# Optimization experiments

Measured on AMD Instinct MI355X. Metric: run time of the kernel, lower is better.

Reference implementation:

```python
import jax, jax.numpy as jnp
import numpy as np

B, N, H, DH, ORDER, DEG = 64, 256, 8, 64, 4, 16
D = H * DH
TOTAL = B * N
E = TOTAL * DEG


def setup_inputs() -> dict:
    key = jax.random.key(0)
    ks = jax.random.split(key, 16)
    output = jax.random.normal(ks[0], (N, B, D), dtype=jnp.float32)
    # attention weights: positive, row-normalized like softmax output
    attn = jax.nn.softmax(jax.random.normal(ks[1], (B, H, N, N), dtype=jnp.float32), axis=-1)
    out_each_head = jax.random.normal(ks[2], (B, N, H, DH), dtype=jnp.float32)
    # random graph edges, endpoints within the same graph (global node ids)
    g = jax.random.randint(ks[3], (E,), 0, B)
    s = g * N + jax.random.randint(ks[4], (E,), 0, N)
    d = g * N + jax.random.randint(ks[5], (E,), 0, N)
    edge_index = jnp.stack([s, d], axis=0).astype(jnp.int64)
    # full graphs, no padding: feature_indices[:,0]=graph id, [:,1]=node pos
    fi = jnp.stack([jnp.repeat(jnp.arange(B), N), jnp.tile(jnp.arange(N), B)], axis=1).astype(jnp.int64)
    batch = fi[:, 0]
    sc = 0.1
    params = dict(
        W_gcn=jax.random.normal(ks[6], (ORDER, ORDER)) * sc,
        b_gcn=jnp.zeros((ORDER,), jnp.float32),
        W_lin=jax.random.normal(ks[7], (ORDER, ORDER)) * sc,
        b_lin=jnp.zeros((ORDER,), jnp.float32),
        W_cheb=jax.random.normal(ks[8], (ORDER, DH, DH)) * sc,
        b_cheb=jnp.zeros((DH,), jnp.float32),
        W_cat=jax.random.normal(ks[9], (2 * D, D)) * sc,
        b_cat=jnp.zeros((D,), jnp.float32),
        gamma=jnp.ones((D,), jnp.float32),
        beta=jnp.zeros((D,), jnp.float32),
    )
    return dict(output=output, attn=attn, out_each_head=out_each_head,
                edge_index=edge_index, feature_indices=fi, batch=batch, **params)


def reference(output, attn, out_each_head, edge_index, feature_indices, batch,
              W_gcn, b_gcn, W_lin, b_lin, W_cheb, b_cheb, W_cat, b_cat, gamma, beta):
    Bn, Hn, Nn, _ = attn.shape
    C = W_gcn.shape[0]
    total = Bn * Nn
    NT = Hn * total

    # ---- get_filter_coefficients: GCN over fully-connected attention graphs ----
    # edge weights are detached in the original (edge_weight.detach())
    A = jax.lax.stop_gradient(attn).transpose(1, 0, 2, 3).reshape(Hn * Bn, Nn, Nn)
    A_hat = A + jnp.eye(Nn, dtype=A.dtype)  # add self loops (weight 1)
    deg = A_hat.sum(axis=1)                 # deg_j = sum_i A_hat[i,j]
    dinv = jnp.where(deg > 0, jax.lax.rsqrt(deg), 0.0)  # (HB, N)
    # x = ones, so x @ W_gcn is a constant row = column sums of W_gcn
    w_row = W_gcn.sum(axis=0)               # (C,)
    s = jnp.einsum('bi,bij->bj', dinv, A_hat) * dinv     # (HB, N)
    x_c = jnp.tanh(s[:, :, None] * w_row + b_gcn)        # (HB, N, C)
    gap = x_c.mean(axis=1)                  # global avg pool per graph (HB, C)
    coeff = gap @ W_lin + b_lin             # (HB, C) rows ordered (head, batch)

    # ---- dynamic Chebyshev filtering per head on the input graph ----
    offsets = (jnp.arange(Hn) * total).astype(edge_index.dtype)
    src = (edge_index[0][None, :] + offsets[:, None]).reshape(-1)
    dst = (edge_index[1][None, :] + offsets[:, None]).reshape(-1)
    deg_n = jax.ops.segment_sum(jnp.ones(src.shape[0], jnp.float32), dst, num_segments=NT)
    dinv_n = jnp.where(deg_n > 0, jax.lax.rsqrt(deg_n), 0.0)
    norm_e = -(dinv_n[src] * dinv_n[dst])   # scaled Laplacian L_hat = -D^-1/2 A D^-1/2

    def prop(x):  # L_hat @ x via gather/scatter
        return jax.ops.segment_sum(norm_e[:, None] * x[src], dst, num_segments=NT)

    # nodes ordered (head, batch, node)
    x0 = out_each_head.transpose(2, 0, 1, 3).reshape(NT, DH)
    batch_all = (batch[None, :] + (jnp.arange(Hn) * Bn)[:, None]).reshape(-1)  # graph id h*B+b
    c_node = coeff[batch_all]               # (NT, ORDER) per-node dynamic coefficients

    T_prev, T_cur = x0, prop(x0)
    acc = c_node[:, 0:1] * (T_prev @ W_cheb[0]) + c_node[:, 1:2] * (T_cur @ W_cheb[1])
    for k in range(2, C):
        T_next = 2.0 * prop(T_cur) - T_prev
        acc = acc + c_node[:, k:k + 1] * (T_next @ W_cheb[k])
        T_prev, T_cur = T_cur, T_next
    acc = acc + b_cheb                      # (NT, DH)

    # regroup heads: (H, B*N, DH) -> (B*N, H*DH), scatter back to (N, B, D)
    filtered = acc.reshape(Hn, total, DH).transpose(1, 0, 2).reshape(total, Hn * DH)
    out_filtered = jnp.zeros_like(output).at[feature_indices[:, 1], feature_indices[:, 0], :].set(filtered)

    # skip connection + linear_cat + final LayerNorm
    out_cat = jnp.concatenate([output, out_filtered], axis=-1)
    out = out_cat @ W_cat + b_cat
    mu = out.mean(axis=-1, keepdims=True)
    var = ((out - mu) ** 2).mean(axis=-1, keepdims=True)
    out = (out - mu) * jax.lax.rsqrt(var + 1e-5) * gamma + beta
    return out
```

## Files before the change

kernel.cpp:

```cpp
#include <hip/hip_runtime.h>
#include <stdint.h>

#define Bq      64
#define Nq      256
#define Hq      8
#define DHq     64
#define TOTALq  16384
#define NTq     131072
#define Dq      512

typedef __attribute__((ext_vector_type(8))) short short8;
typedef __attribute__((ext_vector_type(4))) float floatx4;

__device__ __forceinline__ unsigned short f2bf(float f) {
    union { float f; unsigned int u; } c; c.f = f;
    unsigned int u = c.u;
    return (unsigned short)((u + 0x7fffu + ((u >> 16) & 1u)) >> 16);
}
__device__ __forceinline__ float bf2f(unsigned short u) {
    union { unsigned int u; float f; } c; c.u = ((unsigned int)u) << 16;
    return c.f;
}

__global__ void pscatter_kernel(const int* __restrict__ srcp, const int* __restrict__ dstp,
                                const int* __restrict__ cnt, float* __restrict__ Pf, int E) {
    int e = blockIdx.x * 256 + threadIdx.x;
    if (e >= E) return;
    int s = srcp[e], d = dstp[e];
    int cs = cnt[s], cd = cnt[d];
    float dvs = (cs > 0) ? rsqrtf((float)cs) : 0.0f;
    float dvd = (cd > 0) ? rsqrtf((float)cd) : 0.0f;
    int g = d >> 8;
    atomicAdd(&Pf[((size_t)g << 16) + ((size_t)(d & 255) << 8) + (s & 255)],
              -(dvs * dvd));
}

__global__ void pconv_kernel(const float* __restrict__ Pf, unsigned short* __restrict__ Pb) {
    int i = (blockIdx.x * 256 + threadIdx.x) * 4;
    float4 v = *(const float4*)(Pf + i);
    unsigned int lo = (unsigned int)f2bf(v.x) | ((unsigned int)f2bf(v.y) << 16);
    unsigned int hi = (unsigned int)f2bf(v.z) | ((unsigned int)f2bf(v.w) << 16);
    *(uint2*)(Pb + i) = make_uint2(lo, hi);
}

__global__ __launch_bounds__(512, 1)
void front_kernel(const float* __restrict__ attn,
                  const float* __restrict__ Wg, const float* __restrict__ bg,
                  const float* __restrict__ Wlin, const float* __restrict__ blin,
                  float* __restrict__ coeff,
                  const int* __restrict__ dstp, int* __restrict__ cnt, int E,
                  const float* __restrict__ Wcat, unsigned short* __restrict__ Wt2,
                  const float* __restrict__ Wch, float* __restrict__ WchTf,
                  float* __restrict__ Pf) {
    __shared__ floatx4 part[8][64];
    __shared__ floatx4 dinv4[64];
    const int bid = blockIdx.x;
    const int tid = threadIdx.x;

    if (bid < 512) {
        const int g = bid;
        const int h = g >> 6;
        const int b = g & 63;
        const float* A = attn + ((size_t)(b * Hq + h)) * (Nq * Nq);
        const int rg = tid >> 6;
        const int cv = tid & 63;
        const float* Ap = A + cv * 4;

        floatx4 regs[32];
        floatx4 s1 = (floatx4){0.f, 0.f, 0.f, 0.f};
#pragma unroll
        for (int r = 0; r < 32; ++r) {
            regs[r] = *(const floatx4*)(Ap + (size_t)(rg * 32 + r) * 256);
            s1 += regs[r];
        }
        part[rg][cv] = s1;
        __syncthreads();

        if (tid < 64) {
            floatx4 cs = part[0][tid];
#pragma unroll
            for (int i = 1; i < 8; ++i) cs += part[i][tid];
            floatx4 dv;
#pragma unroll
            for (int i = 0; i < 4; ++i) dv[i] = rsqrtf(cs[i] + 1.0f);
            dinv4[tid] = dv;
        }
        __syncthreads();

        const float* dsc = (const float*)dinv4;
        floatx4 s2 = (floatx4){0.f, 0.f, 0.f, 0.f};
#pragma unroll
        for (int r = 0; r < 32; ++r)
            s2 += dsc[rg * 32 + r] * regs[r];
        part[rg][cv] = s2;
        __syncthreads();

        if (tid < 64) {
            floatx4 ws = part[0][tid];
#pragma unroll
            for (int i = 1; i < 8; ++i) ws += part[i][tid];
            floatx4 dv = dinv4[tid];
            floatx4 sj = (ws + dv) * dv;

            float wr[4], bgl[4];
#pragma unroll
            for (int c = 0; c < 4; ++c) {
                wr[c]  = Wg[0 * 4 + c] + Wg[1 * 4 + c] + Wg[2 * 4 + c] + Wg[3 * 4 + c];
                bgl[c] = bg[c];
            }
            float v[4];
#pragma unroll
            for (int c = 0; c < 4; ++c) {
                v[c] = tanhf(sj[0] * wr[c] + bgl[c]) + tanhf(sj[1] * wr[c] + bgl[c]) +
                       tanhf(sj[2] * wr[c] + bgl[c]) + tanhf(sj[3] * wr[c] + bgl[c]);
#pragma unroll
                for (int o = 32; o >= 1; o >>= 1) v[c] += __shfl_down(v[c], o, 64);
            }
            float g0 = __shfl(v[0], 0, 64), g1 = __shfl(v[1], 0, 64);
            float g2 = __shfl(v[2], 0, 64), g3 = __shfl(v[3], 0, 64);
            if (tid < 4) {
                float r = blin[tid] + (g0 * Wlin[0 * 4 + tid] + g1 * Wlin[1 * 4 + tid] +
                                       g2 * Wlin[2 * 4 + tid] + g3 * Wlin[3 * 4 + tid]) *
                                          (1.0f / 256.0f);
                coeff[g * 4 + tid] = r;
            }
        }
        return;
    }

    const int nbCnt = (E + 511) >> 9;
    if (bid < 512 + nbCnt) {
        int e = (bid - 512) * 512 + tid;
        if (e < E) atomicAdd(&cnt[dstp[e]], 1);
        return;
    }
    if (bid < 512 + nbCnt + 160) {
        int pb = bid - 512 - nbCnt;
        if (pb < 128) {
            int idx = pb * 512 + tid;
            int col = idx & 511;
            int ktq = idx >> 9;
            const float* src = Wcat + (size_t)(ktq * 8) * 512 + col;
            unsigned int pk[4];
#pragma unroll
            for (int q2 = 0; q2 < 4; ++q2) {
                unsigned short a = f2bf(src[(q2 * 2 + 0) * 512]);
                unsigned short b = f2bf(src[(q2 * 2 + 1) * 512]);
                pk[q2] = (unsigned int)a | ((unsigned int)b << 16);
            }
            *(uint4*)(Wt2 + (size_t)idx * 8) = make_uint4(pk[0], pk[1], pk[2], pk[3]);
        } else {
            int idx = (pb - 128) * 512 + tid;
            int k = idx >> 12, rem = idx & 4095;
            int n = rem >> 6, j = rem & 63;
            WchTf[idx] = Wch[(k << 12) + (j << 6) + n];
        }
        return;
    }
    {
        int zb = bid - 512 - nbCnt - 160;
        size_t i = ((size_t)zb * 512 + tid) * 4;
        *(float4*)(Pf + i) = make_float4(0.f, 0.f, 0.f, 0.f);
    }
}

__global__ __launch_bounds__(512, 2)
void cheb_fused(const unsigned short* __restrict__ Pb, const float* __restrict__ oeh,
                const float* __restrict__ WchTf, const float* __restrict__ coeff,
                const float* __restrict__ bch, unsigned short* __restrict__ filtb) {
    extern __shared__ unsigned char sm[];
    unsigned short* cm = (unsigned short*)sm;
    unsigned short* rm = (unsigned short*)(sm + 32768);
    unsigned short* Wl = (unsigned short*)(sm + 65536);

    const int g = blockIdx.x;
    const int b = (g & 7) * 8 + ((g >> 3) & 7);
    const int h = g >> 6;
    const int tid = threadIdx.x;
    const int lane = tid & 63, wv = tid >> 6;
    const int wr = wv >> 1, wc = wv & 1;
    const int quad = lane >> 4, l15 = lane & 15;

    const unsigned short* Pbase = Pb + ((size_t)b << 16);
    const float* cf = coeff + (h * 64 + b) * 4;

    {
        const int sn = tid >> 1;
        const int sh = (tid & 1) * 32;
        const float* sp = oeh + (size_t)(b * 256 + sn) * 512 + h * 64 + sh;
        unsigned int pk[16];
#pragma unroll
        for (int j = 0; j < 8; ++j) {
            float4 v = *(const float4*)(sp + j * 4);
            pk[2 * j]     = (unsigned)f2bf(v.x) | ((unsigned)f2bf(v.y) << 16);
            pk[2 * j + 1] = (unsigned)f2bf(v.z) | ((unsigned)f2bf(v.w) << 16);
        }
#pragma unroll
        for (int jj = 0; jj < 4; ++jj)
            *(uint4*)(rm + sn * 64 + ((((sh >> 3) + jj) ^ (sn & 7)) << 3)) =
                make_uint4(pk[4 * jj], pk[4 * jj + 1], pk[4 * jj + 2], pk[4 * jj + 3]);
#pragma unroll
        for (int e = 0; e < 32; ++e) {
            int c = sh + e;
            unsigned short v =
                (unsigned short)((e & 1) ? (pk[e >> 1] >> 16) : (pk[e >> 1] & 0xffffu));
            cm[c * 256 + (((sn >> 3) ^ (c & 31)) << 3) + (sn & 7)] = v;
        }
        float ck = cf[0];
        int r = tid >> 3, su = tid & 7;
        const float* wp = WchTf + r * 64 + su * 8;
        float4 w0 = *(const float4*)wp, w1 = *(const float4*)(wp + 4);
        *(uint4*)(Wl + r * 72 + su * 8) = make_uint4(
            (unsigned)f2bf(w0.x * ck) | ((unsigned)f2bf(w0.y * ck) << 16),
            (unsigned)f2bf(w0.z * ck) | ((unsigned)f2bf(w0.w * ck) << 16),
            (unsigned)f2bf(w1.x * ck) | ((unsigned)f2bf(w1.y * ck) << 16),
            (unsigned)f2bf(w1.z * ck) | ((unsigned)f2bf(w1.w * ck) << 16));
    }
    __syncthreads();

    unsigned int curp[4][2][2], prvp[4][2][2];
#pragma unroll
    for (int rt = 0; rt < 4; ++rt)
#pragma unroll
        for (int ct = 0; ct < 2; ++ct)
#pragma unroll
            for (int p = 0; p < 2; ++p) {
                int m = wr * 64 + rt * 16 + quad * 4 + 2 * p;
                int c = wc * 32 + ct * 16 + l15;
                curp[rt][ct][p] = *(const unsigned int*)(cm + c * 256 +
                                                         (((m >> 3) ^ (c & 31)) << 3) + (m & 7));
                prvp[rt][ct][p] = 0u;
            }

    floatx4 accf[4][2];
#pragma unroll
    for (int rt = 0; rt < 4; ++rt)
#pragma unroll
        for (int ct = 0; ct < 2; ++ct) accf[rt][ct] = (floatx4){0.f, 0.f, 0.f, 0.f};

#pragma unroll
    for (int k = 0; k < 4; ++k) {
#pragma unroll
        for (int kk = 0; kk < 2; ++kk) {
            short8 af[4], bfw[2];
#pragma unroll
            for (int rt = 0; rt < 4; ++rt) {
                int row = wr * 64 + rt * 16 + l15;
                af[rt] = *(const short8*)(rm + row * 64 + (((kk * 4 + quad) ^ (row & 7)) << 3));
            }
#pragma unroll
            for (int ct = 0; ct < 2; ++ct) {
                int oc = wc * 32 + ct * 16 + l15;
                bfw[ct] = *(const short8*)(Wl + oc * 72 + kk * 32 + quad * 8);
            }
#pragma unroll
            for (int rt = 0; rt < 4; ++rt)
#pragma unroll
                for (int ct = 0; ct < 2; ++ct)
                    accf[rt][ct] = __builtin_amdgcn_mfma_f32_16x16x32_bf16(
                        af[rt], bfw[ct], accf[rt][ct], 0, 0, 0);
        }
        if (k < 3) {
            floatx4 accp[4][2];
#pragma unroll
            for (int rt = 0; rt < 4; ++rt)
#pragma unroll
                for (int ct = 0; ct < 2; ++ct) accp[rt][ct] = (floatx4){0.f, 0.f, 0.f, 0.f};
#pragma unroll
            for (int kt = 0; kt < 8; ++kt) {
                short8 ap[4], bp[2];
#pragma unroll
                for (int rt = 0; rt < 4; ++rt) {
                    int row = wr * 64 + rt * 16 + l15;
                    ap[rt] = *(const short8*)(Pbase + row * 256 + kt * 32 + quad * 8);
                }
#pragma unroll
                for (int ct = 0; ct < 2; ++ct) {
                    int c = wc * 32 + ct * 16 + l15;
                    bp[ct] = *(const short8*)(cm + c * 256 + (((kt * 4 + quad) ^ (c & 31)) << 3));
                }
#pragma unroll
                for (int rt = 0; rt < 4; ++rt)
#pragma unroll
                    for (int ct = 0; ct < 2; ++ct)
                        accp[rt][ct] = __builtin_amdgcn_mfma_f32_16x16x32_bf16(
                            ap[rt], bp[ct], accp[rt][ct], 0, 0, 0);
            }
            __syncthreads();
#pragma unroll
            for (int rt = 0; rt < 4; ++rt)
#pragma unroll
                for (int ct = 0; ct < 2; ++ct)
#pragma unroll
                    for (int p = 0; p < 2; ++p) {
                        float a0 = accp[rt][ct][2 * p], a1 = accp[rt][ct][2 * p + 1];
                        if (k > 0) {
                            unsigned pv = prvp[rt][ct][p];
                            a0 = 2.0f * a0 - bf2f((unsigned short)(pv & 0xffffu));
                            a1 = 2.0f * a1 - bf2f((unsigned short)(pv >> 16));
                        }
                        unsigned nv = (unsigned)f2bf(a0) | ((unsigned)f2bf(a1) << 16);
                        prvp[rt][ct][p] = curp[rt][ct][p];
                        curp[rt][ct][p] = nv;
                        int m = wr * 64 + rt * 16 + quad * 4 + 2 * p;
                        int c = wc * 32 + ct * 16 + l15;
                        if (k < 2)
                            *(unsigned int*)(cm + c * 256 + (((m >> 3) ^ (c & 31)) << 3) +
                                             (m & 7)) = nv;
                        rm[m * 64 + (((c >> 3) ^ (m & 7)) << 3) + (c & 7)] =
                            (unsigned short)(nv & 0xffffu);
                        rm[(m + 1) * 64 + (((c >> 3) ^ ((m + 1) & 7)) << 3) + (c & 7)] =
                            (unsigned short)(nv >> 16);
                    }
            {
                float ck = cf[k + 1];
                int r = tid >> 3, su = tid & 7;
                const float* wp = WchTf + (k + 1) * 4096 + r * 64 + su * 8;
                float4 w0 = *(const float4*)wp, w1 = *(const float4*)(wp + 4);
                *(uint4*)(Wl + r * 72 + su * 8) = make_uint4(
                    (unsigned)f2bf(w0.x * ck) | ((unsigned)f2bf(w0.y * ck) << 16),
                    (unsigned)f2bf(w0.z * ck) | ((unsigned)f2bf(w0.w * ck) << 16),
                    (unsigned)f2bf(w1.x * ck) | ((unsigned)f2bf(w1.y * ck) << 16),
                    (unsigned)f2bf(w1.z * ck) | ((unsigned)f2bf(w1.w * ck) << 16));
            }
            __syncthreads();
        }
    }

    float bias[2];
#pragma unroll
    for (int ct = 0; ct < 2; ++ct) bias[ct] = bch[wc * 32 + ct * 16 + l15];
#pragma unroll
    for (int rt = 0; rt < 4; ++rt)
#pragma unroll
        for (int ct = 0; ct < 2; ++ct) {
            int c = wc * 32 + ct * 16 + l15;
#pragma unroll
            for (int i = 0; i < 4; ++i) {
                int m = wr * 64 + rt * 16 + quad * 4 + i;
                filtb[((size_t)m * 64 + b) * 512 + h * 64 + c] =
                    f2bf(accf[rt][ct][i] + bias[ct]);
            }
        }
}

__global__ __launch_bounds__(512, 2)
void gemm_ln_mfma(const float* __restrict__ outp, const unsigned short* __restrict__ filtb,
                  const unsigned short* __restrict__ Wt2, const float* __restrict__ bcat,
                  const float* __restrict__ gamma, const float* __restrict__ beta,
                  float* __restrict__ out) {
    extern __shared__ unsigned char smc[];
    unsigned short* A_lds0 = (unsigned short*)smc;
    unsigned short* A_lds1 = (unsigned short*)(smc + 4096);
    float* ep = (float*)smc;

    const int tid = threadIdx.x;
    const int lane = tid & 63;
    const int wv = tid >> 6;
    const int quad = lane >> 4;
    const int l15 = lane & 15;
    const int r0 = blockIdx.x * 64;

    const int s_row = tid >> 3;
    const int s_sub = tid & 7;
    const int s_q   = s_sub >> 1;
    const int s_e   = (s_sub & 1) * 4;

    const size_t boff = (size_t)(quad * 512 + wv * 64 + l15) * 8;

    floatx4 acc[4][4];
#pragma unroll
    for (int rt = 0; rt < 4; ++rt)
#pragma unroll
        for (int ct = 0; ct < 4; ++ct) acc[rt][ct] = (floatx4){0.f, 0.f, 0.f, 0.f};

    short8 bA[4], bB[4];
    float4 avX_f, avY_f;
    uint2  avX_b, avY_b;

    {
#pragma unroll
        for (int ct = 0; ct < 4; ++ct)
            bA[ct] = *(const short8*)(Wt2 + boff + ct * 128);
#pragma unroll
        for (int ct = 0; ct < 4; ++ct)
            bB[ct] = *(const short8*)(Wt2 + (size_t)16384 + boff + ct * 128);
        float4 av = *(const float4*)(outp + (size_t)(r0 + s_row) * 512 + s_sub * 4);
        avY_f = *(const float4*)(outp + (size_t)(r0 + s_row) * 512 + 32 + s_sub * 4);
        uint2 ap;
        ap.x = (unsigned int)f2bf(av.x) | ((unsigned int)f2bf(av.y) << 16);
        ap.y = (unsigned int)f2bf(av.z) | ((unsigned int)f2bf(av.w) << 16);
        *(uint2*)(A_lds0 + (s_q * 64 + s_row) * 8 + s_e) = ap;
        __syncthreads();
    }

#define GSTEP(KT, BCUR, AC, AN, AVCF, AVCB, AVNF, AVNB)                             \
    do {                                                                            \
        const int kt_ = (KT);                                                       \
        if (kt_ <= 29) {                                                            \
            const int kc2_ = (kt_ + 2) * 32;                                        \
            if (kc2_ < 512)                                                         \
                AVNF = *(const float4*)(outp + (size_t)(r0 + s_row) * 512 +         \
                                        kc2_ + s_sub * 4);                          \
            else                                                                    \
                AVNB = *(const uint2*)(filtb + (size_t)(r0 + s_row) * 512 +         \
                                       (kc2_ - 512) + s_sub * 4);                   \
        }                                                                           \
        short8 af_[4];                                                              \
        _Pragma("unroll")                                                           \
        for (int rt = 0; rt < 4; ++rt)                                              \
            af_[rt] = *(const short8*)(AC + (quad * 64 + rt * 16 + l15) * 8);       \
        _Pragma("unroll")                                                           \
        for (int rt = 0; rt < 4; ++rt)                                              \
            _Pragma("unroll")                                                       \
            for (int ct = 0; ct < 4; ++ct)                                          \
                acc[rt][ct] = __builtin_amdgcn_mfma_f32_16x16x32_bf16(              \
                    af_[rt], BCUR[ct], acc[rt][ct], 0, 0, 0);                       \
        if (kt_ <= 29) {                                                            \
            _Pragma("unroll")                                                       \
            for (int ct = 0; ct < 4; ++ct)                                          \
                BCUR[ct] = *(const short8*)(Wt2 + (size_t)(kt_ + 2) * 16384 +       \
                                            boff + ct * 128);                       \
        }                                                                           \
        if (kt_ <= 30) {                                                            \
            uint2 ap_;                                                              \
            if ((kt_ + 1) * 32 < 512) {                                             \
                ap_.x = (unsigned int)f2bf(AVCF.x) | ((unsigned int)f2bf(AVCF.y) << 16); \
                ap_.y = (unsigned int)f2bf(AVCF.z) | ((unsigned int)f2bf(AVCF.w) << 16); \
            } else {                                                                \
                ap_ = AVCB;                                                         \
            }                                                                       \
            *(uint2*)(AN + (s_q * 64 + s_row) * 8 + s_e) = ap_;                     \
        }                                                                           \
        asm volatile("s_waitcnt lgkmcnt(0)" ::: "memory");                          \
        __builtin_amdgcn_s_barrier();                                               \
        __builtin_amdgcn_sched_barrier(0);                                          \
    } while (0)

    for (int kt2 = 0; kt2 < 16; ++kt2) {
        GSTEP(2 * kt2,     bA, A_lds0, A_lds1, avY_f, avY_b, avX_f, avX_b);
        GSTEP(2 * kt2 + 1, bB, A_lds1, A_lds0, avX_f, avX_b, avY_f, avY_b);
    }
#undef GSTEP

    float gg[8], bb[8];
#pragma unroll
    for (int i = 0; i < 8; ++i) { gg[i] = gamma[i * 64 + lane]; bb[i] = beta[i * 64 + lane]; }
    float bc[4];
#pragma unroll
    for (int ct = 0; ct < 4; ++ct) bc[ct] = bcat[wv * 64 + ct * 16 + l15];

    for (int half = 0; half < 2; ++half) {
        __syncthreads();
#pragma unroll
        for (int rt2 = 0; rt2 < 2; ++rt2) {
            const int rt = half * 2 + rt2;
#pragma unroll
            for (int ct = 0; ct < 4; ++ct) {
                const int col = wv * 64 + ct * 16 + l15;
#pragma unroll
                for (int i = 0; i < 4; ++i) {
                    const int row_l = rt2 * 16 + quad * 4 + i;
                    ep[row_l * 512 + col] = acc[rt][ct][i] + bc[ct];
                }
            }
        }
        __syncthreads();
#pragma unroll
        for (int m4 = 0; m4 < 4; ++m4) {
            const int m = wv * 4 + m4;
            float s = 0.0f, ss = 0.0f;
#pragma unroll
            for (int i = 0; i < 8; ++i) {
                float v = ep[m * 512 + i * 64 + lane];
                s += v; ss += v * v;
            }
#pragma unroll
            for (int o = 32; o >= 1; o >>= 1) {
                s += __shfl_down(s, o, 64);
                ss += __shfl_down(ss, o, 64);
            }
            s = __shfl(s, 0, 64);
            ss = __shfl(ss, 0, 64);
            const float mu = s * (1.0f / 512.0f);
            const float var = ss * (1.0f / 512.0f) - mu * mu;
            const float rs = rsqrtf(var + 1e-5f);
            const int r = r0 + half * 32 + m;
#pragma unroll
            for (int i = 0; i < 8; ++i) {
                const int d = i * 64 + lane;
                out[(size_t)r * 512 + d] = (ep[m * 512 + d] - mu) * rs * gg[i] + bb[i];
            }
        }
    }
}

extern "C" void kernel_launch(void* const* d_in, const int* in_sizes, int n_in,
                              void* d_out, int out_size, void* d_ws, size_t ws_size,
                              hipStream_t stream) {
    const float* output       = (const float*)d_in[0];
    const float* attn         = (const float*)d_in[1];
    const float* oeh          = (const float*)d_in[2];
    const int*   edge_index   = (const int*)d_in[3];
    const float* W_gcn        = (const float*)d_in[6];
    const float* b_gcn        = (const float*)d_in[7];
    const float* W_lin        = (const float*)d_in[8];
    const float* b_lin        = (const float*)d_in[9];
    const float* W_cheb       = (const float*)d_in[10];
    const float* b_cheb       = (const float*)d_in[11];
    const float* W_cat        = (const float*)d_in[12];
    const float* b_cat        = (const float*)d_in[13];
    const float* gamma        = (const float*)d_in[14];
    const float* beta         = (const float*)d_in[15];
    float* out = (float*)d_out;

    const int E = in_sizes[3] / 2;
    const int* srcp = edge_index;
    const int* dstp = edge_index + E;

    uint8_t* ws = (uint8_t*)d_ws;
    size_t cur = 0;
    auto alloc = [&](size_t bytes) -> void* {
        void* p = ws + cur;
        cur += (bytes + 255) & ~(size_t)255;
        return p;
    };
    int*   cnt     = (int*)alloc(TOTALq * sizeof(int));
    float* Pf      = (float*)alloc((size_t)64 * 65536 * sizeof(float));
    unsigned short* Pb   = (unsigned short*)alloc((size_t)64 * 65536 * 2);
    float* coeff   = (float*)alloc(512 * 4 * sizeof(float));
    float* WchTf   = (float*)alloc(4 * 64 * 64 * sizeof(float));
    unsigned short* Wt2  = (unsigned short*)alloc((size_t)Dq * 1024 * 2);
    unsigned short* filtb = (unsigned short*)alloc((size_t)TOTALq * Dq * 2);
    (void)ws_size; (void)n_in; (void)out_size;

    hipMemsetAsync(cnt, 0, TOTALq * sizeof(int), stream);

    const int nbCnt = (E + 511) / 512;
    const int frontGrid = 512 + nbCnt + 160 + 2048;
    front_kernel<<<frontGrid, 512, 0, stream>>>(attn, W_gcn, b_gcn, W_lin, b_lin, coeff,
                                                dstp, cnt, E, W_cat, Wt2, W_cheb, WchTf,
                                                Pf);

    pscatter_kernel<<<(E + 255) / 256, 256, 0, stream>>>(srcp, dstp, cnt, Pf, E);
    pconv_kernel<<<4096, 256, 0, stream>>>(Pf, Pb);

    cheb_fused<<<512, 512, 74752, stream>>>(Pb, oeh, WchTf, coeff, b_cheb, filtb);

    gemm_ln_mfma<<<TOTALq / 64, 512, 65536, stream>>>(output, filtb, Wt2, b_cat,
                                                      gamma, beta, out);
}
```

Baseline: 381.4 us.

## Raise cheb_fused occupancy, prefetch P tiles, and reload cur state from LDS

Raises the launch bound from 2 to 4 blocks per CU to force lower register use. To make room it drops the curp register array and reloads the current Chebyshev term from the cm shared buffer. It also double-buffers the global loads of the P adjacency tiles two k-steps ahead so they overlap the MFMAs. The risks are register spills under the tighter bound and the LDS footprint (~74KB+ per block), which may stop 4 blocks from fitting on a CU anyway.

```diff
diff --git a/kernel.cpp b/kernel.cpp
--- a/kernel.cpp
+++ b/kernel.cpp
@@ -164,7 +164,7 @@
     }
 }
 
-__global__ __launch_bounds__(512, 2)
+__global__ __launch_bounds__(512, 4)
 void cheb_fused(const unsigned short* __restrict__ Pb, const float* __restrict__ oeh,
                 const float* __restrict__ WchTf, const float* __restrict__ coeff,
                 const float* __restrict__ bch, unsigned short* __restrict__ filtb) {
@@ -182,6 +182,7 @@
     const int quad = lane >> 4, l15 = lane & 15;
 
     const unsigned short* Pbase = Pb + ((size_t)b << 16);
+    const unsigned short* Prow = Pbase + (size_t)(wr * 64 + l15) * 256 + quad * 8;
     const float* cf = coeff + (h * 64 + b) * 4;
 
     {
@@ -218,19 +219,13 @@
     }
     __syncthreads();
 
-    unsigned int curp[4][2][2], prvp[4][2][2];
+    unsigned int prvp[4][2][2];
 #pragma unroll
     for (int rt = 0; rt < 4; ++rt)
 #pragma unroll
         for (int ct = 0; ct < 2; ++ct)
 #pragma unroll
-            for (int p = 0; p < 2; ++p) {
-                int m = wr * 64 + rt * 16 + quad * 4 + 2 * p;
-                int c = wc * 32 + ct * 16 + l15;
-                curp[rt][ct][p] = *(const unsigned int*)(cm + c * 256 +
-                                                         (((m >> 3) ^ (c & 31)) << 3) + (m & 7));
-                prvp[rt][ct][p] = 0u;
-            }
+            for (int p = 0; p < 2; ++p) prvp[rt][ct][p] = 0u;
 
     floatx4 accf[4][2];
 #pragma unroll
@@ -240,6 +235,15 @@
 
 #pragma unroll
     for (int k = 0; k < 4; ++k) {
+        short8 paA[4], paB[4];
+        if (k < 3) {
+#pragma unroll
+            for (int rt = 0; rt < 4; ++rt)
+                paA[rt] = *(const short8*)(Prow + rt * 16 * 256);
+#pragma unroll
+            for (int rt = 0; rt < 4; ++rt)
+                paB[rt] = *(const short8*)(Prow + rt * 16 * 256 + 32);
+        }
 #pragma unroll
         for (int kk = 0; kk < 2; ++kk) {
             short8 af[4], bfw[2];
@@ -266,26 +270,35 @@
             for (int rt = 0; rt < 4; ++rt)
 #pragma unroll
                 for (int ct = 0; ct < 2; ++ct) accp[rt][ct] = (floatx4){0.f, 0.f, 0.f, 0.f};
-#pragma unroll
-            for (int kt = 0; kt < 8; ++kt) {
-                short8 ap[4], bp[2];
-#pragma unroll
-                for (int rt = 0; rt < 4; ++rt) {
-                    int row = wr * 64 + rt * 16 + l15;
-                    ap[rt] = *(const short8*)(Pbase + row * 256 + kt * 32 + quad * 8);
-                }
-#pragma unroll
-                for (int ct = 0; ct < 2; ++ct) {
-                    int c = wc * 32 + ct * 16 + l15;
-                    bp[ct] = *(const short8*)(cm + c * 256 + (((kt * 4 + quad) ^ (c & 31)) << 3));
-                }
-#pragma unroll
-                for (int rt = 0; rt < 4; ++rt)
-#pragma unroll
-                    for (int ct = 0; ct < 2; ++ct)
-                        accp[rt][ct] = __builtin_amdgcn_mfma_f32_16x16x32_bf16(
-                            ap[rt], bp[ct], accp[rt][ct], 0, 0, 0);
-            }
+
+#define PSTEP(KT, CUR)                                                              \
+    do {                                                                            \
+        short8 bp_[2];                                                              \
+        _Pragma("unroll")                                                           \
+        for (int ct = 0; ct < 2; ++ct) {                                            \
+            int c = wc * 32 + ct * 16 + l15;                                        \
+            bp_[ct] = *(const short8*)(cm + c * 256 +                               \
+                                       ((((KT) * 4 + quad) ^ (c & 31)) << 3));      \
+        }                                                                           \
+        _Pragma("unroll")                                                           \
+        for (int rt = 0; rt < 4; ++rt)                                              \
+            _Pragma("unroll")                                                       \
+            for (int ct = 0; ct < 2; ++ct)                                          \
+                accp[rt][ct] = __builtin_amdgcn_mfma_f32_16x16x32_bf16(             \
+                    CUR[rt], bp_[ct], accp[rt][ct], 0, 0, 0);                       \
+        if ((KT) + 2 < 8) {                                                         \
+            _Pragma("unroll")                                                       \
+            for (int rt = 0; rt < 4; ++rt)                                          \
+                CUR[rt] = *(const short8*)(Prow + rt * 16 * 256 + ((KT) + 2) * 32); \
+        }                                                                           \
+    } while (0)
+
+            PSTEP(0, paA); PSTEP(1, paB);
+            PSTEP(2, paA); PSTEP(3, paB);
+            PSTEP(4, paA); PSTEP(5, paB);
+            PSTEP(6, paA); PSTEP(7, paB);
+#undef PSTEP
+
             __syncthreads();
 #pragma unroll
             for (int rt = 0; rt < 4; ++rt)
@@ -293,6 +306,12 @@
                 for (int ct = 0; ct < 2; ++ct)
 #pragma unroll
                     for (int p = 0; p < 2; ++p) {
+                        int m = wr * 64 + rt * 16 + quad * 4 + 2 * p;
+                        int c = wc * 32 + ct * 16 + l15;
+                        unsigned int* cmSlot =
+                            (unsigned int*)(cm + c * 256 + (((m >> 3) ^ (c & 31)) << 3) +
+                                            (m & 7));
+                        unsigned cur = *cmSlot;
                         float a0 = accp[rt][ct][2 * p], a1 = accp[rt][ct][2 * p + 1];
                         if (k > 0) {
                             unsigned pv = prvp[rt][ct][p];
@@ -300,13 +319,9 @@
                             a1 = 2.0f * a1 - bf2f((unsigned short)(pv >> 16));
                         }
                         unsigned nv = (unsigned)f2bf(a0) | ((unsigned)f2bf(a1) << 16);
-                        prvp[rt][ct][p] = curp[rt][ct][p];
-                        curp[rt][ct][p] = nv;
-                        int m = wr * 64 + rt * 16 + quad * 4 + 2 * p;
-                        int c = wc * 32 + ct * 16 + l15;
+                        prvp[rt][ct][p] = cur;
                         if (k < 2)
-                            *(unsigned int*)(cm + c * 256 + (((m >> 3) ^ (c & 31)) << 3) +
-                                             (m & 7)) = nv;
+                            *cmSlot = nv;
                         rm[m * 64 + (((c >> 3) ^ (m & 7)) << 3) + (c & 7)] =
                             (unsigned short)(nv & 0xffffu);
                         rm[(m + 1) * 64 + (((c >> 3) ^ ((m + 1) & 7)) << 3) + (c & 7)] =
```

Measured after the change: 390.5 us. 1.02x slower.
